# Kernel tuning notes

Measured on AMD Instinct MI355X. Metric: run time of the kernel, lower is better.

Reference implementation:

```python
import jax, jax.numpy as jnp
import numpy as np

LOW, HIGH = 0.1, 0.3
HYST_ITERS = 16  # fixed-point iterations for hysteresis flood-fill

_GAUSS = jnp.array([[1., 2., 1.], [2., 4., 2.], [1., 2., 1.]], jnp.float32) / 16.0
_SOBEL_X = jnp.array([[-1., 0., 1.], [-2., 0., 2.], [-1., 0., 1.]], jnp.float32)
_SOBEL_Y = jnp.array([[-1., -2., -1.], [0., 0., 0.], [1., 2., 1.]], jnp.float32)


def _conv3x3(x, k):
    # x: [B,H,W,1], k: [3,3] -> SAME conv, stride 1
    return jax.lax.conv_general_dilated(
        x, k.reshape(3, 3, 1, 1), (1, 1), 'SAME',
        dimension_numbers=('NHWC', 'HWIO', 'NHWC'))


def _shift(x, dh, dw):
    # result[b,i,j,c] = x[b,i+dh,j+dw,c], zeros outside the image
    p = jnp.pad(x, ((0, 0), (1, 1), (1, 1), (0, 0)))
    return jax.lax.dynamic_slice(p, (0, 1 + dh, 1 + dw, 0), x.shape)


def setup_inputs() -> dict:
    key = jax.random.key(0)
    inputs = jax.random.uniform(key, (8, 1024, 1024, 1), dtype=jnp.float32)
    return {"inputs": inputs}


def reference(inputs) -> jnp.ndarray:
    # 1) Gaussian blur + Sobel gradients
    blurred = _conv3x3(inputs, _GAUSS)
    gx = _conv3x3(blurred, _SOBEL_X)
    gy = _conv3x3(blurred, _SOBEL_Y)
    mag = jnp.sqrt(gx * gx + gy * gy)
    direction = jnp.arctan2(gy, gx)

    # 2) Non-maximum suppression keyed on quantized gradient direction
    angle = direction * (180.0 / np.pi)
    angle = jnp.where(angle < 0, angle + 180.0, angle)
    b0 = (angle < 22.5) | (angle >= 157.5)          # horizontal gradient -> left/right
    b1 = (angle >= 22.5) & (angle < 67.5)           # 45 deg diagonal
    b2 = (angle >= 67.5) & (angle < 112.5)          # vertical -> up/down
    # b3 (135 deg) is the fallback branch
    n1 = jnp.where(b0, _shift(mag, 0, 1),
         jnp.where(b1, _shift(mag, -1, 1),
         jnp.where(b2, _shift(mag, -1, 0), _shift(mag, -1, -1))))
    n2 = jnp.where(b0, _shift(mag, 0, -1),
         jnp.where(b1, _shift(mag, 1, -1),
         jnp.where(b2, _shift(mag, 1, 0), _shift(mag, 1, 1))))
    suppressed = jnp.where((mag >= n1) & (mag >= n2), mag, 0.0)

    # 3) Double threshold
    strong = jnp.where(suppressed >= HIGH, 1.0, 0.0)
    weak = jnp.where((suppressed >= LOW) & (suppressed < HIGH), 1.0, 0.0)

    # 4) Hysteresis: propagate strong edges through weak pixels (iterated 3x3 dilation)
    def body(i, edges):
        dil = jax.lax.reduce_window(edges, -jnp.inf, jax.lax.max,
                                    (1, 3, 3, 1), (1, 1, 1, 1), 'SAME')
        return jnp.maximum(edges, weak * (dil > 0).astype(edges.dtype))

    edges = jax.lax.fori_loop(0, HYST_ITERS, body, strong)
    return edges
```

## Files before the change

### kernel.cpp

```cpp
#include <hip/hip_runtime.h>
#include <math.h>
#include <stdint.h>

typedef unsigned long long u64;

#define HH 1024
#define WW 1024
#define NB 8
#define WPR 16

__device__ __forceinline__ float blur_at(const float* p) {
#pragma clang fp contract(off)
    float s = p[0] * 0.0625f;
    s += p[1] * 0.125f;
    s += p[2] * 0.0625f;
    s += p[70] * 0.125f;
    s += p[71] * 0.25f;
    s += p[72] * 0.125f;
    s += p[140] * 0.0625f;
    s += p[141] * 0.125f;
    s += p[142] * 0.0625f;
    return s;
}

__device__ __forceinline__ void sobel_at(const float* p, float& osx, float& osy) {
#pragma clang fp contract(off)
    float x00 = p[0], x01 = p[1], x02 = p[2];
    float x10 = p[68], x12 = p[70];
    float x20 = p[136], x21 = p[137], x22 = p[138];
    float gx = -x00;
    gx += x02;
    gx -= 2.f * x10;
    gx += 2.f * x12;
    gx -= x20;
    gx += x22;
    float gy = -x00;
    gy -= 2.f * x01;
    gy -= x02;
    gy += x20;
    gy += 2.f * x21;
    gy += x22;
    osx = gx;
    osy = gy;
}

__global__ __launch_bounds__(256) void canny_s1(const float* __restrict__ in,
                                                u64* __restrict__ strongB,
                                                u64* __restrict__ weakB) {
#pragma clang fp contract(off)
    const int bx  = blockIdx.x;
    const int b   = bx >> 8;
    const int rem = bx & 255;
    const int y0  = (rem >> 4) << 6;
    const int x0  = (rem & 15) << 6;
    const float* img = in + (size_t)b * (HH * WW);

    __shared__ float sIn[70 * 70];
    __shared__ float sBl[68 * 68];
    float* sMag = sIn;

    const int tid = threadIdx.x;

    for (int idx = tid; idx < 70 * 70; idx += 256) {
        int r = idx / 70, c = idx - r * 70;
        int gy = y0 - 3 + r, gx = x0 - 3 + c;
        float v = 0.f;
        if ((unsigned)gy < HH && (unsigned)gx < WW) v = img[gy * WW + gx];
        sIn[idx] = v;
    }
    __syncthreads();

    for (int idx = tid; idx < 68 * 68; idx += 256) {
        int r = idx / 68, c = idx - r * 68;
        int gy = y0 - 2 + r, gx = x0 - 2 + c;
        float v = 0.f;
        if ((unsigned)gy < HH && (unsigned)gx < WW) v = blur_at(&sIn[r * 70 + c]);
        sBl[idx] = v;
    }
    __syncthreads();

    for (int idx = tid; idx < 66 * 66; idx += 256) {
        int r = idx / 66, c = idx - r * 66;
        int gy = y0 - 1 + r, gx = x0 - 1 + c;
        float v = 0.f;
        if ((unsigned)gy < HH && (unsigned)gx < WW) {
            float sx, sy;
            sobel_at(&sBl[r * 68 + c], sx, sy);
            float xx = sx * sx;
            float yy = sy * sy;
            v = sqrtf(xx + yy);
        }
        sMag[r * 66 + c] = v;
    }
    __syncthreads();

    const int lane = tid & 63;
    const int wv   = tid >> 6;

    for (int y = wv; y < 64; y += 4) {
        float sx, sy;
        sobel_at(&sBl[(y + 1) * 68 + (lane + 1)], sx, sy);

        const int base = (y + 1) * 66 + (lane + 1);
        float m = sMag[base];

        float ang = (float)atan2((double)sy, (double)sx);
        float deg = ang * 57.29577951308232f;
        if (deg < 0.f) deg += 180.f;

        float n1, n2;
        if (deg < 22.5f || deg >= 157.5f) {
            n1 = sMag[base + 1];      n2 = sMag[base - 1];
        } else if (deg < 67.5f) {
            n1 = sMag[base - 66 + 1]; n2 = sMag[base + 66 - 1];
        } else if (deg < 112.5f) {
            n1 = sMag[base - 66];     n2 = sMag[base + 66];
        } else {
            n1 = sMag[base - 66 - 1]; n2 = sMag[base + 66 + 1];
        }

        bool keep = (m >= n1) && (m >= n2);
        bool st = keep && (m >= 0.3f);
        bool wk = keep && (m >= 0.1f) && (m < 0.3f);

        u64 bs = __ballot(st);
        u64 bw = __ballot(wk);
        if (lane == 0) {
            size_t o = (size_t)(b * HH + y0 + y) * WPR + (x0 >> 6);
            strongB[o] = bs;
            weakB[o]   = bw;
        }
    }
}

__global__ __launch_bounds__(256) void canny_s2(const u64* __restrict__ strongB,
                                                const u64* __restrict__ weakB,
                                                float* __restrict__ out) {
    const int bx  = blockIdx.x;
    const int b   = bx >> 8;
    const int rem = bx & 255;
    const int y0  = (rem >> 4) << 6;
    const int x0  = (rem & 15) << 6;
    const int w0  = (x0 >> 6) - 1;

    __shared__ u64 sE[2][96][3];
    __shared__ u64 sW[96][3];

    const int tid = threadIdx.x;

    for (int idx = tid; idx < 96 * 3; idx += 256) {
        int r = idx / 3, w = idx - r * 3;
        int gy = y0 - 16 + r, gw = w0 + w;
        u64 s = 0, k = 0;
        if ((unsigned)gy < HH && (unsigned)gw < WPR) {
            size_t o = (size_t)(b * HH + gy) * WPR + gw;
            s = strongB[o];
            k = weakB[o];
        }
        sE[0][r][w] = s;
        sW[r][w]    = k;
    }
    __syncthreads();

    for (int it = 0; it < 16; ++it) {
        const u64 (*src)[3] = sE[it & 1];
        u64 (*dst)[3]       = sE[(it & 1) ^ 1];
        for (int idx = tid; idx < 96 * 3; idx += 256) {
            int r = idx / 3, w = idx - r * 3;
            u64 dil = 0;
#pragma unroll
            for (int dr = -1; dr <= 1; ++dr) {
                int rr = r + dr;
                if ((unsigned)rr < 96u) {
                    u64 mid = src[rr][w];
                    u64 lft = (w > 0) ? src[rr][w - 1] : 0ull;
                    u64 rgt = (w < 2) ? src[rr][w + 1] : 0ull;
                    dil |= mid | (mid << 1) | (mid >> 1) | (lft >> 63) | (rgt << 63);
                }
            }
            dst[r][w] = src[r][w] | (sW[r][w] & dil);
        }
        __syncthreads();
    }

    const int lane = tid & 63;
    const int wv   = tid >> 6;
    for (int y = wv; y < 64; y += 4) {
        u64 word = sE[0][y + 16][1];
        out[(size_t)(b * HH + y0 + y) * WW + x0 + lane] = ((word >> lane) & 1ull) ? 1.f : 0.f;
    }
}

extern "C" void kernel_launch(void* const* d_in, const int* in_sizes, int n_in,
                              void* d_out, int out_size, void* d_ws, size_t ws_size,
                              hipStream_t stream) {
    const float* in = (const float*)d_in[0];
    float* out = (float*)d_out;

    u64* strongB = (u64*)d_ws;
    u64* weakB   = strongB + (size_t)NB * HH * WPR;

    dim3 grid(NB * 16 * 16);
    canny_s1<<<grid, 256, 0, stream>>>(in, strongB, weakB);
    canny_s2<<<grid, 256, 0, stream>>>(strongB, weakB, out);
}
```

Measured before the change: 162.9 us.

## Replace atan2 with tangent-ratio bucketing and run hysteresis per-wave in registers

In stage one, the double-precision atan2 used for direction quantization is replaced by comparisons of |gy| against tan(22.5°)·|gx| and tan(67.5°)·|gx|. Values near a boundary fall back to the exact atan2 path, which keeps the buckets bit-identical to before. In stage two, each 64x64 tile's hysteresis is handled by one wave instead of a block: rows live in registers, vertical neighbours come from shuffles, and the shared-memory syncs go away. Output rows are written with float4 stores, though each lane now writes whole rows, so the store pattern is strided per lane.

Result: faster. 147.4 us (-9.5%).

```diff
diff --git a/kernel.cpp b/kernel.cpp
--- a/kernel.cpp
+++ b/kernel.cpp
@@ -44,6 +44,17 @@
     osy = gy;
 }
 
+__device__ __forceinline__ int bucket_exact(float sy, float sx) {
+#pragma clang fp contract(off)
+    float ang = (float)atan2((double)sy, (double)sx);
+    float deg = ang * 57.29577951308232f;
+    if (deg < 0.f) deg += 180.f;
+    if (deg < 22.5f || deg >= 157.5f) return 0;
+    if (deg < 67.5f) return 1;
+    if (deg < 112.5f) return 2;
+    return 3;
+}
+
 __global__ __launch_bounds__(256) void canny_s1(const float* __restrict__ in,
                                                 u64* __restrict__ strongB,
                                                 u64* __restrict__ weakB) {
@@ -104,20 +115,28 @@
         const int base = (y + 1) * 66 + (lane + 1);
         float m = sMag[base];
 
-        float ang = (float)atan2((double)sy, (double)sx);
-        float deg = ang * 57.29577951308232f;
-        if (deg < 0.f) deg += 180.f;
+        const float t1 = 0.41421356237309503f;
+        const float t2 = 2.414213562373095f;
+        float ax = fabsf(sx), ay = fabsf(sy);
+        float r1 = t1 * ax, r2 = t2 * ax;
+        int bucket;
+        bool near1 = fabsf(ay - r1) <= 1e-4f * (ay + r1);
+        bool near2 = fabsf(ay - r2) <= 1e-4f * (ay + r2);
+        if (near1 | near2) {
+            bucket = bucket_exact(sy, sx);
+        } else if (ay < r1) {
+            bucket = 0;
+        } else if (ay < r2) {
+            bucket = ((sx > 0.f) == (sy > 0.f)) ? 1 : 3;
+        } else {
+            bucket = 2;
+        }
 
         float n1, n2;
-        if (deg < 22.5f || deg >= 157.5f) {
-            n1 = sMag[base + 1];      n2 = sMag[base - 1];
-        } else if (deg < 67.5f) {
-            n1 = sMag[base - 66 + 1]; n2 = sMag[base + 66 - 1];
-        } else if (deg < 112.5f) {
-            n1 = sMag[base - 66];     n2 = sMag[base + 66];
-        } else {
-            n1 = sMag[base - 66 - 1]; n2 = sMag[base + 66 + 1];
-        }
+        if (bucket == 0)      { n1 = sMag[base + 1];      n2 = sMag[base - 1]; }
+        else if (bucket == 1) { n1 = sMag[base - 66 + 1]; n2 = sMag[base + 66 - 1]; }
+        else if (bucket == 2) { n1 = sMag[base - 66];     n2 = sMag[base + 66]; }
+        else                  { n1 = sMag[base - 66 - 1]; n2 = sMag[base + 66 + 1]; }
 
         bool keep = (m >= n1) && (m >= n2);
         bool st = keep && (m >= 0.3f);
@@ -136,58 +155,73 @@
 __global__ __launch_bounds__(256) void canny_s2(const u64* __restrict__ strongB,
                                                 const u64* __restrict__ weakB,
                                                 float* __restrict__ out) {
-    const int bx  = blockIdx.x;
-    const int b   = bx >> 8;
-    const int rem = bx & 255;
+    const int wave = threadIdx.x >> 6;
+    const int lane = threadIdx.x & 63;
+    const int tile = blockIdx.x * 4 + wave;
+    const int b   = tile >> 8;
+    const int rem = tile & 255;
     const int y0  = (rem >> 4) << 6;
     const int x0  = (rem & 15) << 6;
     const int w0  = (x0 >> 6) - 1;
 
-    __shared__ u64 sE[2][96][3];
-    __shared__ u64 sW[96][3];
-
-    const int tid = threadIdx.x;
-
-    for (int idx = tid; idx < 96 * 3; idx += 256) {
-        int r = idx / 3, w = idx - r * 3;
-        int gy = y0 - 16 + r, gw = w0 + w;
-        u64 s = 0, k = 0;
-        if ((unsigned)gy < HH && (unsigned)gw < WPR) {
-            size_t o = (size_t)(b * HH + gy) * WPR + gw;
-            s = strongB[o];
-            k = weakB[o];
-        }
-        sE[0][r][w] = s;
-        sW[r][w]    = k;
-    }
-    __syncthreads();
+    u64 e[2][3], k[2][3];
+#pragma unroll
+    for (int i = 0; i < 2; ++i) {
+        int rr = 2 * lane + i;
+        int gy = y0 - 16 + rr;
+#pragma unroll
+        for (int w = 0; w < 3; ++w) {
+            int gw = w0 + w;
+            u64 s = 0, kk = 0;
+            if (rr < 96 && (unsigned)gy < HH && (unsigned)gw < WPR) {
+                size_t o = (size_t)(b * HH + gy) * WPR + gw;
+                s  = strongB[o];
+                kk = weakB[o];
+            }
+            e[i][w] = s;
+            k[i][w] = kk;
+        }
+    }
 
     for (int it = 0; it < 16; ++it) {
-        const u64 (*src)[3] = sE[it & 1];
-        u64 (*dst)[3]       = sE[(it & 1) ^ 1];
-        for (int idx = tid; idx < 96 * 3; idx += 256) {
-            int r = idx / 3, w = idx - r * 3;
-            u64 dil = 0;
-#pragma unroll
-            for (int dr = -1; dr <= 1; ++dr) {
-                int rr = r + dr;
-                if ((unsigned)rr < 96u) {
-                    u64 mid = src[rr][w];
-                    u64 lft = (w > 0) ? src[rr][w - 1] : 0ull;
-                    u64 rgt = (w < 2) ? src[rr][w + 1] : 0ull;
-                    dil |= mid | (mid << 1) | (mid >> 1) | (lft >> 63) | (rgt << 63);
-                }
+        u64 hd[2][3];
+#pragma unroll
+        for (int i = 0; i < 2; ++i)
+#pragma unroll
+            for (int w = 0; w < 3; ++w) {
+                u64 m = e[i][w];
+                u64 l = (w > 0) ? e[i][w - 1] : 0ull;
+                u64 r = (w < 2) ? e[i][w + 1] : 0ull;
+                hd[i][w] = m | (m << 1) | (m >> 1) | (l >> 63) | (r << 63);
             }
-            dst[r][w] = src[r][w] | (sW[r][w] & dil);
-        }
-        __syncthreads();
-    }
-
-    const int lane = tid & 63;
-    const int wv   = tid >> 6;
-    for (int y = wv; y < 64; y += 4) {
-        u64 word = sE[0][y + 16][1];
-        out[(size_t)(b * HH + y0 + y) * WW + x0 + lane] = ((word >> lane) & 1ull) ? 1.f : 0.f;
+#pragma unroll
+        for (int w = 0; w < 3; ++w) {
+            u64 up = (u64)__shfl_up((long long)hd[1][w], 1);
+            if (lane == 0) up = 0ull;
+            u64 dn = (u64)__shfl_down((long long)hd[0][w], 1);
+            if (lane == 63) dn = 0ull;
+            u64 d0 = up | hd[0][w] | hd[1][w];
+            u64 d1 = hd[0][w] | hd[1][w] | dn;
+            e[0][w] |= k[0][w] & d0;
+            e[1][w] |= k[1][w] & d1;
+        }
+    }
+
+    if (lane >= 8 && lane < 40) {
+#pragma unroll
+        for (int i = 0; i < 2; ++i) {
+            int gy = y0 - 16 + 2 * lane + i;
+            u64 word = e[i][1];
+            float* orow = out + (size_t)(b * HH + gy) * WW + x0;
+            for (int c = 0; c < 64; c += 4) {
+                float4 v;
+                v.x = ((word >> c) & 1ull)       ? 1.f : 0.f;
+                v.y = ((word >> (c + 1)) & 1ull) ? 1.f : 0.f;
+                v.z = ((word >> (c + 2)) & 1ull) ? 1.f : 0.f;
+                v.w = ((word >> (c + 3)) & 1ull) ? 1.f : 0.f;
+                *reinterpret_cast<float4*>(orow + c) = v;
+            }
+        }
     }
 }
 
@@ -200,7 +234,6 @@
     u64* strongB = (u64*)d_ws;
     u64* weakB   = strongB + (size_t)NB * HH * WPR;
 
-    dim3 grid(NB * 16 * 16);
-    canny_s1<<<grid, 256, 0, stream>>>(in, strongB, weakB);
-    canny_s2<<<grid, 256, 0, stream>>>(strongB, weakB, out);
-}
+    canny_s1<<<dim3(NB * 16 * 16), 256, 0, stream>>>(in, strongB, weakB);
+    canny_s2<<<dim3(NB * 16 * 16 / 4), 256, 0, stream>>>(strongB, weakB, out);
+}
```
